# Optimization experiments

Measured on AMD Instinct MI355X. Metric: run time of the kernel, lower is better.

## Reference

```python
import jax, jax.numpy as jnp
import numpy as np

N_NODES, N_EDGES, NNZ, F_IN, HID, K = 50000, 10000, 800000, 128, 512, 10


def setup_inputs() -> dict:
    key = jax.random.key(0)
    ks = jax.random.split(key, 6)
    x = jax.random.normal(ks[0], (N_NODES, F_IN), dtype=jnp.float32)
    node_idx = jax.random.randint(ks[1], (NNZ,), 0, N_NODES)
    edge_idx = jax.random.randint(ks[2], (NNZ,), 0, N_EDGES)
    hyperedge_index = jnp.stack([node_idx, edge_idx]).astype(jnp.int64)
    edge_weight = jax.random.uniform(ks[3], (N_EDGES,), dtype=jnp.float32, minval=0.5, maxval=1.5)
    theta = jax.random.normal(ks[4], (K + 1,), dtype=jnp.float32) * 0.1
    lin1_w = jax.random.normal(ks[5], (HID, F_IN), dtype=jnp.float32) * (1.0 / np.sqrt(F_IN))
    lin1_b = jnp.zeros((HID,), dtype=jnp.float32)
    return {"x": x, "hyperedge_index": hyperedge_index, "edge_weight": edge_weight,
            "theta": theta, "lin1_w": lin1_w, "lin1_b": lin1_b}


def _hyper_prop_factory(node_idx, edge_idx, edge_weight, n_nodes, n_edges):
    """Returns A_norm @ x where A_norm = Dv^-1/2 H W De^-1 H^T Dv^-1/2."""
    ones = jnp.ones_like(node_idx, dtype=edge_weight.dtype)
    d_e = jax.ops.segment_sum(ones, edge_idx, num_segments=n_edges)            # edge degree
    d_v = jax.ops.segment_sum(edge_weight[edge_idx], node_idx, num_segments=n_nodes)
    dv_is = jnp.where(d_v > 0, jax.lax.rsqrt(jnp.maximum(d_v, 1e-12)), 0.0)
    de_w = edge_weight * jnp.where(d_e > 0, 1.0 / jnp.maximum(d_e, 1e-12), 0.0)

    def prop(x):
        xv = x * dv_is[:, None]                                               # [N, F]
        m_e = jax.ops.segment_sum(xv[node_idx], edge_idx, num_segments=n_edges)
        m_e = m_e * de_w[:, None]                                             # [E, F]
        out = jax.ops.segment_sum(m_e[edge_idx], node_idx, num_segments=n_nodes)
        return out * dv_is[:, None]

    return prop


def cheb_hypergraph(x, node_idx, edge_idx, edge_weight, theta, n_nodes, n_edges):
    # L_tilde = L - I = -A_norm (lambda_max = 2). Chebyshev recurrence on L_tilde.
    prop = _hyper_prop_factory(node_idx, edge_idx, edge_weight, n_nodes, n_edges)
    t_prev = x                       # T_0
    out = theta[0] * t_prev
    t_cur = -prop(x)                 # T_1 = L_tilde x
    out = out + theta[1] * t_cur
    for k in range(2, theta.shape[0]):
        t_next = -2.0 * prop(t_cur) - t_prev   # T_k = 2 L_tilde T_{k-1} - T_{k-2}
        out = out + theta[k] * t_next
        t_prev, t_cur = t_cur, t_next
    return out


def reference(x, hyperedge_index, edge_weight, theta, lin1_w, lin1_b):
    node_idx = hyperedge_index[0]
    edge_idx = hyperedge_index[1]
    n_nodes = x.shape[0]
    n_edges = edge_weight.shape[0]
    # eval mode: both dropouts are identity
    h = cheb_hypergraph(x, node_idx, edge_idx, edge_weight, theta, n_nodes, n_edges)
    h = jnp.einsum('nf,hf->nh', h, lin1_w) + lin1_b
    # is_bns=False -> no batch norm; act_fn='relu'
    return jax.nn.relu(h)
```

## Files before the change

kernel.cpp:

```cpp
#include <hip/hip_runtime.h>


#define N_NODES 50000
#define N_EDGES 10000
#define NNZ     800000
#define F_IN    128
#define HID     512
#define F4      (F_IN / 4)
#define R16     16

typedef __attribute__((ext_vector_type(8))) short bf16x8;
typedef __attribute__((ext_vector_type(4))) float f32x4;

static __device__ __forceinline__ unsigned short f2bf(float f) {
    union { float f; unsigned u; } c; c.f = f;
    unsigned u = c.u;
    unsigned r = (u + 0x7fffu + ((u >> 16) & 1u)) >> 16;
    return (unsigned short)r;
}
static __device__ __forceinline__ float blo(unsigned u) {
    union { unsigned u; float f; } c; c.u = u << 16; return c.f;
}
static __device__ __forceinline__ float bhi(unsigned u) {
    union { unsigned u; float f; } c; c.u = u & 0xffff0000u; return c.f;
}
static __device__ __forceinline__ unsigned pack2(float lo, float hi) {
    return (unsigned)f2bf(lo) | ((unsigned)f2bf(hi) << 16);
}

__global__ void k_zero8(int* __restrict__ cnt8_e, int* __restrict__ cnt8_n) {
    int i = blockIdx.x * blockDim.x + threadIdx.x;
    if (i < 8 * N_NODES) cnt8_n[i] = 0;
    if (i < 8 * N_EDGES) cnt8_e[i] = 0;
}

__global__ void k_degrees(const int* __restrict__ hidx,
                          int* __restrict__ cnt8_e,
                          int* __restrict__ cnt8_n,
                          int* __restrict__ rank_e,
                          int* __restrict__ rank_v) {
    int i = blockIdx.x * blockDim.x + threadIdx.x;
    if (i >= NNZ) return;
    int xcd = (int)blockIdx.x & 7;
    int v = hidx[i];
    int e = hidx[NNZ + i];
    v = min(max(v, 0), N_NODES - 1);
    e = min(max(e, 0), N_EDGES - 1);
    int re = atomicAdd(&cnt8_e[xcd * N_EDGES + e], 1);
    int rv = atomicAdd(&cnt8_n[xcd * N_NODES + v], 1);
    rank_e[i] = re | (xcd << 24);
    rank_v[i] = rv | (xcd << 24);
}

__global__ void k_off8(int* __restrict__ cnt8_e,
                       int* __restrict__ cnt8_n,
                       int* __restrict__ counts_e,
                       int* __restrict__ counts_n) {
    int i = blockIdx.x * blockDim.x + threadIdx.x;
    if (i < N_EDGES) {
        int s = 0;
#pragma unroll
        for (int x = 0; x < 8; ++x) {
            int c = cnt8_e[x * N_EDGES + i];
            cnt8_e[x * N_EDGES + i] = s;
            s += c;
        }
        counts_e[i] = s;
    }
    if (i < N_NODES) {
        int s = 0;
#pragma unroll
        for (int x = 0; x < 8; ++x) {
            int c = cnt8_n[x * N_NODES + i];
            cnt8_n[x * N_NODES + i] = s;
            s += c;
        }
        counts_n[i] = s;
    }
}

__global__ __launch_bounds__(1024) void k_scan_blk(const int* __restrict__ counts, int n,
                                                   int stride,
                                                   int* __restrict__ out,
                                                   int* __restrict__ partial) {
    __shared__ int sd[1024];
    int tid = (int)threadIdx.x;
    int i = blockIdx.x * 1024 + tid;
    int v = (i < n) ? counts[(size_t)i * stride] : 0;
    sd[tid] = v;
    __syncthreads();
    for (int off = 1; off < 1024; off <<= 1) {
        int t = (tid >= off) ? sd[tid - off] : 0;
        __syncthreads();
        sd[tid] += t;
        __syncthreads();
    }
    if (i < n) out[i] = sd[tid] - v;
    if (tid == 1023) partial[blockIdx.x] = sd[1023];
}

__global__ void k_scan_top(int* __restrict__ partial, int nb, int* __restrict__ total_out) {
    int lane = (int)threadIdx.x;
    int v = (lane < nb) ? partial[lane] : 0;
    int incl = v;
    for (int off = 1; off < 64; off <<= 1) {
        int t = __shfl_up(incl, off);
        if (lane >= off) incl += t;
    }
    if (lane < nb) partial[lane] = incl - v;
    if (lane == 63) *total_out = incl;
}

__global__ __launch_bounds__(1024) void k_scan_add(int* __restrict__ out, int n,
                                                   const int* __restrict__ partial) {
    int i = blockIdx.x * 1024 + (int)threadIdx.x;
    if (i < n) out[i] += partial[blockIdx.x];
}

__global__ void k_fill(const int* __restrict__ hidx,
                       const int* __restrict__ edge_ptr,
                       const int* __restrict__ node_ptr,
                       const int* __restrict__ rank_e,
                       const int* __restrict__ rank_v,
                       const int* __restrict__ off8_e,
                       const int* __restrict__ off8_n,
                       int* __restrict__ edge_node,
                       int* __restrict__ node_edge) {
    int i = blockIdx.x * blockDim.x + threadIdx.x;
    if (i >= NNZ) return;
    int v = hidx[i];
    int e = hidx[NNZ + i];
    v = min(max(v, 0), N_NODES - 1);
    e = min(max(e, 0), N_EDGES - 1);
    int pe = rank_e[i];
    int pv = rank_v[i];
    int xe = pe >> 24, re = pe & 0xFFFFFF;
    int xv = pv >> 24, rv = pv & 0xFFFFFF;
    edge_node[edge_ptr[e] + off8_e[xe * N_EDGES + e] + re] = v;
    node_edge[node_ptr[v] + off8_n[xv * N_NODES + v] + rv] = e;
}

__global__ void k_norms2(const float* __restrict__ ew,
                         const int* __restrict__ edge_ptr,
                         const int* __restrict__ node_ptr,
                         const int* __restrict__ node_edge,
                         float* __restrict__ dv_is,
                         float* __restrict__ de_w) {
    int i = blockIdx.x * blockDim.x + threadIdx.x;
    if (i < N_NODES) {
        int s = node_ptr[i], t = node_ptr[i + 1];
        float d = 0.f;
        for (int j = s; j < t; ++j) d += ew[node_edge[j]];
        dv_is[i] = (d > 0.f) ? rsqrtf(fmaxf(d, 1e-12f)) : 0.f;
    }
    if (i < N_EDGES) {
        int c = edge_ptr[i + 1] - edge_ptr[i];
        de_w[i] = ew[i] * ((c > 0) ? (1.f / (float)c) : 0.f);
    }
}

__global__ void k_init(const float* __restrict__ x,
                       const float* __restrict__ theta,
                       const float* __restrict__ dv_is,
                       uint4* __restrict__ bufA,
                       float* __restrict__ acc) {
    int i = blockIdx.x * blockDim.x + threadIdx.x;
    if (i >= N_NODES * R16) return;
    int v = i >> 4;
    float dvv = dv_is[v];
    float w = (dvv > 0.f) ? dvv : 1.f;
    float4 x0 = ((const float4*)x)[2 * i];
    float4 x1 = ((const float4*)x)[2 * i + 1];
    uint4 q;
    q.x = pack2(w * x0.x, w * x0.y); q.y = pack2(w * x0.z, w * x0.w);
    q.z = pack2(w * x1.x, w * x1.y); q.w = pack2(w * x1.z, w * x1.w);
    bufA[i] = q;
    float t0 = theta[0];
    float4 a0, a1;
    a0.x = t0 * x0.x; a0.y = t0 * x0.y; a0.z = t0 * x0.z; a0.w = t0 * x0.w;
    a1.x = t0 * x1.x; a1.y = t0 * x1.y; a1.z = t0 * x1.z; a1.w = t0 * x1.w;
    ((float4*)acc)[2 * i]     = a0;
    ((float4*)acc)[2 * i + 1] = a1;
}

__global__ void k_phaseA(const uint4* __restrict__ tin,
                         const float* __restrict__ de_w,
                         const int* __restrict__ edge_ptr,
                         const int* __restrict__ edge_node,
                         uint4* __restrict__ m_e) {
    int g      = threadIdx.x >> 5;
    int stream = (threadIdx.x >> 4) & 1;
    int lane   = threadIdx.x & 15;
    int e = blockIdx.x * 8 + g;
    int s = edge_ptr[e], t = edge_ptr[e + 1];
    float a0=0.f,a1=0.f,a2=0.f,a3=0.f,a4=0.f,a5=0.f,a6=0.f,a7=0.f;
    int j = s + stream;
    for (; j + 6 < t; j += 8) {
        int v0 = edge_node[j];
        int v1 = edge_node[j + 2];
        int v2 = edge_node[j + 4];
        int v3 = edge_node[j + 6];
        uint4 q0 = tin[v0 * R16 + lane];
        uint4 q1 = tin[v1 * R16 + lane];
        uint4 q2 = tin[v2 * R16 + lane];
        uint4 q3 = tin[v3 * R16 + lane];
        a0 += (blo(q0.x) + blo(q1.x)) + (blo(q2.x) + blo(q3.x));
        a1 += (bhi(q0.x) + bhi(q1.x)) + (bhi(q2.x) + bhi(q3.x));
        a2 += (blo(q0.y) + blo(q1.y)) + (blo(q2.y) + blo(q3.y));
        a3 += (bhi(q0.y) + bhi(q1.y)) + (bhi(q2.y) + bhi(q3.y));
        a4 += (blo(q0.z) + blo(q1.z)) + (blo(q2.z) + blo(q3.z));
        a5 += (bhi(q0.z) + bhi(q1.z)) + (bhi(q2.z) + bhi(q3.z));
        a6 += (blo(q0.w) + blo(q1.w)) + (blo(q2.w) + blo(q3.w));
        a7 += (bhi(q0.w) + bhi(q1.w)) + (bhi(q2.w) + bhi(q3.w));
    }
    for (; j < t; j += 2) {
        int v0 = edge_node[j];
        uint4 q0 = tin[v0 * R16 + lane];
        a0 += blo(q0.x); a1 += bhi(q0.x);
        a2 += blo(q0.y); a3 += bhi(q0.y);
        a4 += blo(q0.z); a5 += bhi(q0.z);
        a6 += blo(q0.w); a7 += bhi(q0.w);
    }
    a0 += __shfl_xor(a0, 16); a1 += __shfl_xor(a1, 16);
    a2 += __shfl_xor(a2, 16); a3 += __shfl_xor(a3, 16);
    a4 += __shfl_xor(a4, 16); a5 += __shfl_xor(a5, 16);
    a6 += __shfl_xor(a6, 16); a7 += __shfl_xor(a7, 16);
    if (stream == 0) {
        float w = de_w[e];
        uint4 o;
        o.x = pack2(a0 * w, a1 * w); o.y = pack2(a2 * w, a3 * w);
        o.z = pack2(a4 * w, a5 * w); o.w = pack2(a6 * w, a7 * w);
        m_e[e * R16 + lane] = o;
    }
}

__global__ void k_phaseB(const uint4* __restrict__ m_e,
                         const float* __restrict__ dv_is,
                         const int* __restrict__ node_ptr,
                         const int* __restrict__ node_edge,
                         uint4* __restrict__ tio,
                         float* __restrict__ acc,
                         const float* __restrict__ theta, int k,
                         float ca, float cb) {
    int g      = threadIdx.x >> 5;
    int stream = (threadIdx.x >> 4) & 1;
    int lane   = threadIdx.x & 15;
    int v = blockIdx.x * 8 + g;
    int s = node_ptr[v], t = node_ptr[v + 1];
    float s0=0.f,s1=0.f,s2=0.f,s3=0.f,s4=0.f,s5=0.f,s6=0.f,s7=0.f;
    int j = s + stream;
    for (; j + 2 < t; j += 4) {
        int e0 = node_edge[j];
        int e1 = node_edge[j + 2];
        uint4 q0 = m_e[e0 * R16 + lane];
        uint4 q1 = m_e[e1 * R16 + lane];
        s0 += blo(q0.x) + blo(q1.x); s1 += bhi(q0.x) + bhi(q1.x);
        s2 += blo(q0.y) + blo(q1.y); s3 += bhi(q0.y) + bhi(q1.y);
        s4 += blo(q0.z) + blo(q1.z); s5 += bhi(q0.z) + bhi(q1.z);
        s6 += blo(q0.w) + blo(q1.w); s7 += bhi(q0.w) + bhi(q1.w);
    }
    if (j < t) {
        int e0 = node_edge[j];
        uint4 q0 = m_e[e0 * R16 + lane];
        s0 += blo(q0.x); s1 += bhi(q0.x);
        s2 += blo(q0.y); s3 += bhi(q0.y);
        s4 += blo(q0.z); s5 += bhi(q0.z);
        s6 += blo(q0.w); s7 += bhi(q0.w);
    }
    s0 += __shfl_xor(s0, 16); s1 += __shfl_xor(s1, 16);
    s2 += __shfl_xor(s2, 16); s3 += __shfl_xor(s3, 16);
    s4 += __shfl_xor(s4, 16); s5 += __shfl_xor(s5, 16);
    s6 += __shfl_xor(s6, 16); s7 += __shfl_xor(s7, 16);
    if (stream == 0) {
        float dvv = dv_is[v];
        float scf = ca * dvv * dvv;
        float iw  = (dvv > 0.f) ? (1.f / dvv) : 1.f;
        float thinv = theta[k] * iw;
        int idx = v * R16 + lane;
        uint4 tp = tio[idx];
        float t0 = scf * s0 + cb * blo(tp.x);
        float t1 = scf * s1 + cb * bhi(tp.x);
        float t2 = scf * s2 + cb * blo(tp.y);
        float t3 = scf * s3 + cb * bhi(tp.y);
        float t4 = scf * s4 + cb * blo(tp.z);
        float t5 = scf * s5 + cb * bhi(tp.z);
        float t6 = scf * s6 + cb * blo(tp.w);
        float t7 = scf * s7 + cb * bhi(tp.w);
        uint4 tn;
        tn.x = pack2(t0, t1); tn.y = pack2(t2, t3);
        tn.z = pack2(t4, t5); tn.w = pack2(t6, t7);
        tio[idx] = tn;
        float4* acc4 = (float4*)acc;
        int ai = v * 32 + lane * 2;
        float4 a = acc4[ai];
        a.x += thinv * t0; a.y += thinv * t1; a.z += thinv * t2; a.w += thinv * t3;
        acc4[ai] = a;
        float4 b = acc4[ai + 1];
        b.x += thinv * t4; b.y += thinv * t5; b.z += thinv * t6; b.w += thinv * t7;
        acc4[ai + 1] = b;
    }
}

#define M_TILES 782
__global__ __launch_bounds__(256) void k_gemm(const float* __restrict__ A,
                                              const float* __restrict__ W,
                                              const float* __restrict__ bias,
                                              float* __restrict__ out) {
    __shared__ short Asm[64 * 136];
    __shared__ short Wsm[64 * 136];
    int id  = (int)blockIdx.x;
    int xcd = id & 7;
    int sub = id >> 3;
    int h_t = sub & 7;
    int m_i = sub >> 3;
    int m_t = xcd * 98 + m_i;
    if (m_t >= M_TILES) return;
    int m0 = m_t * 64;
    int h0 = h_t * 64;
    int tid = (int)threadIdx.x;

    const float4* A4 = (const float4*)A;
    const float4* W4 = (const float4*)W;
#pragma unroll
    for (int i = 0; i < 4; ++i) {
        int c   = tid + i * 256;
        int row = c >> 4;
        int q4  = c & 15;
        int gr = m0 + row;
        float4 a0, a1;
        if (gr < N_NODES) {
            a0 = A4[(size_t)gr * 32 + q4 * 2];
            a1 = A4[(size_t)gr * 32 + q4 * 2 + 1];
        } else {
            a0 = make_float4(0.f, 0.f, 0.f, 0.f);
            a1 = a0;
        }
        uint4 pa;
        pa.x = pack2(a0.x, a0.y); pa.y = pack2(a0.z, a0.w);
        pa.z = pack2(a1.x, a1.y); pa.w = pack2(a1.z, a1.w);
        *(uint4*)&Asm[row * 136 + q4 * 8] = pa;
        float4 w0 = W4[(size_t)(h0 + row) * 32 + q4 * 2];
        float4 w1 = W4[(size_t)(h0 + row) * 32 + q4 * 2 + 1];
        uint4 pw;
        pw.x = pack2(w0.x, w0.y); pw.y = pack2(w0.z, w0.w);
        pw.z = pack2(w1.x, w1.y); pw.w = pack2(w1.z, w1.w);
        *(uint4*)&Wsm[row * 136 + q4 * 8] = pw;
    }
    __syncthreads();

    int lane = tid & 63;
    int wv   = tid >> 6;
    int l16  = lane & 15;
    int quad = lane >> 4;

    f32x4 acc[4];
#pragma unroll
    for (int n = 0; n < 4; ++n) acc[n] = (f32x4){0.f, 0.f, 0.f, 0.f};

#pragma unroll
    for (int ks = 0; ks < 4; ++ks) {
        int k0 = ks * 32;
        bf16x8 af = *(const bf16x8*)&Asm[(wv * 16 + l16) * 136 + k0 + quad * 8];
#pragma unroll
        for (int n = 0; n < 4; ++n) {
            bf16x8 bf = *(const bf16x8*)&Wsm[(n * 16 + l16) * 136 + k0 + quad * 8];
            acc[n] = __builtin_amdgcn_mfma_f32_16x16x32_bf16(af, bf, acc[n], 0, 0, 0);
        }
    }

#pragma unroll
    for (int n = 0; n < 4; ++n) {
        float bb = bias[h0 + n * 16 + l16];
#pragma unroll
        for (int r = 0; r < 4; ++r) {
            int gr = m0 + wv * 16 + quad * 4 + r;
            if (gr < N_NODES)
                out[(size_t)gr * HID + h0 + n * 16 + l16] =
                    fmaxf(acc[n][r] + bb, 0.f);
        }
    }
}

extern "C" void kernel_launch(void* const* d_in, const int* in_sizes, int n_in,
                              void* d_out, int out_size, void* d_ws, size_t ws_size,
                              hipStream_t stream) {
    const float* x     = (const float*)d_in[0];
    const int*   hidx  = (const int*)d_in[1];
    const float* ew    = (const float*)d_in[2];
    const float* theta = (const float*)d_in[3];
    const float* w1    = (const float*)d_in[4];
    const float* b1    = (const float*)d_in[5];
    float*       out   = (float*)d_out;
    int kp1 = in_sizes[3];

    char* ob = (char*)d_out;
    size_t oo = 0;
    auto oalloc = [&](size_t bytes) -> void* {
        void* p = ob + oo;
        oo = (oo + bytes + 255) & ~(size_t)255;
        return p;
    };
    uint4* bufA      = (uint4*)oalloc((size_t)N_NODES * F_IN * 2);
    uint4* bufB      = (uint4*)oalloc((size_t)N_NODES * F_IN * 2);
    uint4* m_e       = (uint4*)oalloc((size_t)N_EDGES * F_IN * 2);
    int*   edge_node = (int*)oalloc((size_t)NNZ * 4);
    int*   node_edge = (int*)oalloc((size_t)NNZ * 4);
    int*   rank_e    = (int*)oalloc((size_t)NNZ * 4);
    int*   rank_v    = (int*)oalloc((size_t)NNZ * 4);
    int*   cnt8_e    = (int*)oalloc((size_t)8 * N_EDGES * 4);
    int*   cnt8_n    = (int*)oalloc((size_t)8 * N_NODES * 4);
    int*   counts_e  = (int*)oalloc((size_t)N_EDGES * 4);
    int*   counts_n  = (int*)oalloc((size_t)N_NODES * 4);

    char* ws = (char*)d_ws;
    size_t off = 0;
    auto alloc = [&](size_t bytes) -> void* {
        void* p = ws + off;
        off = (off + bytes + 255) & ~(size_t)255;
        return p;
    };
    float* accv     = (float*)alloc((size_t)N_NODES * F_IN * 4);
    float* dv_is    = (float*)alloc((size_t)N_NODES * 4);
    float* de_w     = (float*)alloc((size_t)N_EDGES * 4);
    int*   edge_ptr = (int*)alloc((size_t)(N_EDGES + 1) * 4);
    int*   node_ptr = (int*)alloc((size_t)(N_NODES + 1) * 4);
    int*   part_e   = (int*)alloc(64 * 4);
    int*   part_n   = (int*)alloc(64 * 4);

    const int NB_E = (N_EDGES + 1023) / 1024;
    const int NB_N = (N_NODES + 1023) / 1024;

    k_zero8<<<(8 * N_NODES + 255) / 256, 256, 0, stream>>>(cnt8_e, cnt8_n);
    k_degrees<<<(NNZ + 255) / 256, 256, 0, stream>>>(hidx, cnt8_e, cnt8_n, rank_e, rank_v);
    k_off8<<<(N_NODES + 255) / 256, 256, 0, stream>>>(cnt8_e, cnt8_n, counts_e, counts_n);

    k_scan_blk<<<NB_E, 1024, 0, stream>>>(counts_e, N_EDGES, 1, edge_ptr, part_e);
    k_scan_top<<<1, 64, 0, stream>>>(part_e, NB_E, edge_ptr + N_EDGES);
    k_scan_add<<<NB_E, 1024, 0, stream>>>(edge_ptr, N_EDGES, part_e);

    k_scan_blk<<<NB_N, 1024, 0, stream>>>(counts_n, N_NODES, 1, node_ptr, part_n);
    k_scan_top<<<1, 64, 0, stream>>>(part_n, NB_N, node_ptr + N_NODES);
    k_scan_add<<<NB_N, 1024, 0, stream>>>(node_ptr, N_NODES, part_n);

    k_fill<<<(NNZ + 255) / 256, 256, 0, stream>>>(hidx, edge_ptr, node_ptr,
                                                  rank_e, rank_v, cnt8_e, cnt8_n,
                                                  edge_node, node_edge);
    k_norms2<<<(N_NODES + 255) / 256, 256, 0, stream>>>(ew, edge_ptr, node_ptr,
                                                        node_edge, dv_is, de_w);
    k_init<<<(N_NODES * R16 + 255) / 256, 256, 0, stream>>>(x, theta, dv_is, bufA, accv);

    for (int k = 1; k < kp1; ++k) {
        const uint4* tin = (k & 1) ? bufA : bufB;
        uint4*       tio = (k & 1) ? bufB : bufA;
        float ca = (k == 1) ? -1.f : -2.f;
        float cb = (k == 1) ? 0.f : -1.f;
        k_phaseA<<<N_EDGES / 8, 256, 0, stream>>>(tin, de_w, edge_ptr, edge_node, m_e);
        k_phaseB<<<N_NODES / 8, 256, 0, stream>>>(m_e, dv_is, node_ptr, node_edge,
                                                  tio, accv, theta, k, ca, cb);
    }

    k_gemm<<<8 * 98 * 8, 256, 0, stream>>>(accv, w1, b1, out);
}
```

Baseline: 796.3 us.

## Batch Chebyshev accumulator updates every three steps, widen phaseA, merge scans

The fp32 accumulator read-modify-write in phaseB now runs only every third Chebyshev step, plus the final step. It folds theta-weighted contributions of the current, previous (tin) and pre-previous (tio before overwrite) bf16 terms, which removes about two thirds of the full-size accumulator traffic. phaseA now assigns 64 threads (four interleaved streams) per hyperedge instead of 32, adding a second shuffle reduction, to raise memory-level parallelism per edge. The separate edge and node prefix-scan kernels are merged into single launches to cut launch overhead. The trade-off is that older terms are accumulated from bf16-rounded values rather than fp32, a small precision change.

```diff
diff --git a/kernel.cpp b/kernel.cpp
--- a/kernel.cpp
+++ b/kernel.cpp
@@ -8,6 +8,8 @@
 #define HID     512
 #define F4      (F_IN / 4)
 #define R16     16
+#define NB_E    10
+#define NB_N    49
 
 typedef __attribute__((ext_vector_type(8))) short bf16x8;
 typedef __attribute__((ext_vector_type(4))) float f32x4;
@@ -79,14 +81,20 @@
     }
 }
 
-__global__ __launch_bounds__(1024) void k_scan_blk(const int* __restrict__ counts, int n,
-                                                   int stride,
-                                                   int* __restrict__ out,
-                                                   int* __restrict__ partial) {
+__global__ __launch_bounds__(1024) void k_scan_blk2(const int* __restrict__ ce,
+                                                    const int* __restrict__ cn,
+                                                    int* __restrict__ oute,
+                                                    int* __restrict__ outn,
+                                                    int* __restrict__ pe,
+                                                    int* __restrict__ pn) {
     __shared__ int sd[1024];
+    int b = (int)blockIdx.x;
+    const int* counts; int n; int* out; int* partial; int lb;
+    if (b < NB_E) { counts = ce; n = N_EDGES; out = oute; partial = pe; lb = b; }
+    else          { counts = cn; n = N_NODES; out = outn; partial = pn; lb = b - NB_E; }
     int tid = (int)threadIdx.x;
-    int i = blockIdx.x * 1024 + tid;
-    int v = (i < n) ? counts[(size_t)i * stride] : 0;
+    int i = lb * 1024 + tid;
+    int v = (i < n) ? counts[i] : 0;
     sd[tid] = v;
     __syncthreads();
     for (int off = 1; off < 1024; off <<= 1) {
@@ -96,11 +104,16 @@
         __syncthreads();
     }
     if (i < n) out[i] = sd[tid] - v;
-    if (tid == 1023) partial[blockIdx.x] = sd[1023];
-}
-
-__global__ void k_scan_top(int* __restrict__ partial, int nb, int* __restrict__ total_out) {
-    int lane = (int)threadIdx.x;
+    if (tid == 1023) partial[lb] = sd[1023];
+}
+
+__global__ void k_scan_top2(int* __restrict__ pe, int* __restrict__ pn,
+                            int* __restrict__ tot_e, int* __restrict__ tot_n) {
+    int w = (int)threadIdx.x >> 6;
+    int lane = (int)threadIdx.x & 63;
+    int* partial = w ? pn : pe;
+    int nb       = w ? NB_N : NB_E;
+    int* total   = w ? tot_n : tot_e;
     int v = (lane < nb) ? partial[lane] : 0;
     int incl = v;
     for (int off = 1; off < 64; off <<= 1) {
@@ -108,13 +121,19 @@
         if (lane >= off) incl += t;
     }
     if (lane < nb) partial[lane] = incl - v;
-    if (lane == 63) *total_out = incl;
-}
-
-__global__ __launch_bounds__(1024) void k_scan_add(int* __restrict__ out, int n,
-                                                   const int* __restrict__ partial) {
-    int i = blockIdx.x * 1024 + (int)threadIdx.x;
-    if (i < n) out[i] += partial[blockIdx.x];
+    if (lane == 63) *total = incl;
+}
+
+__global__ __launch_bounds__(1024) void k_scan_add2(int* __restrict__ oute,
+                                                    int* __restrict__ outn,
+                                                    const int* __restrict__ pe,
+                                                    const int* __restrict__ pn) {
+    int b = (int)blockIdx.x;
+    int* out; const int* partial; int n; int lb;
+    if (b < NB_E) { out = oute; partial = pe; n = N_EDGES; lb = b; }
+    else          { out = outn; partial = pn; n = N_NODES; lb = b - NB_E; }
+    int i = lb * 1024 + (int)threadIdx.x;
+    if (i < n) out[i] += partial[lb];
 }
 
 __global__ void k_fill(const int* __restrict__ hidx,
@@ -188,18 +207,20 @@
                          const int* __restrict__ edge_ptr,
                          const int* __restrict__ edge_node,
                          uint4* __restrict__ m_e) {
-    int g      = threadIdx.x >> 5;
-    int stream = (threadIdx.x >> 4) & 1;
-    int lane   = threadIdx.x & 15;
-    int e = blockIdx.x * 8 + g;
+    int tid    = (int)threadIdx.x;
+    int g      = tid >> 6;
+    int l64    = tid & 63;
+    int stream = l64 >> 4;
+    int lane   = l64 & 15;
+    int e = blockIdx.x * 4 + g;
     int s = edge_ptr[e], t = edge_ptr[e + 1];
     float a0=0.f,a1=0.f,a2=0.f,a3=0.f,a4=0.f,a5=0.f,a6=0.f,a7=0.f;
     int j = s + stream;
-    for (; j + 6 < t; j += 8) {
+    for (; j + 12 < t; j += 16) {
         int v0 = edge_node[j];
-        int v1 = edge_node[j + 2];
-        int v2 = edge_node[j + 4];
-        int v3 = edge_node[j + 6];
+        int v1 = edge_node[j + 4];
+        int v2 = edge_node[j + 8];
+        int v3 = edge_node[j + 12];
         uint4 q0 = tin[v0 * R16 + lane];
         uint4 q1 = tin[v1 * R16 + lane];
         uint4 q2 = tin[v2 * R16 + lane];
@@ -213,7 +234,7 @@
         a6 += (blo(q0.w) + blo(q1.w)) + (blo(q2.w) + blo(q3.w));
         a7 += (bhi(q0.w) + bhi(q1.w)) + (bhi(q2.w) + bhi(q3.w));
     }
-    for (; j < t; j += 2) {
+    for (; j < t; j += 4) {
         int v0 = edge_node[j];
         uint4 q0 = tin[v0 * R16 + lane];
         a0 += blo(q0.x); a1 += bhi(q0.x);
@@ -225,6 +246,10 @@
     a2 += __shfl_xor(a2, 16); a3 += __shfl_xor(a3, 16);
     a4 += __shfl_xor(a4, 16); a5 += __shfl_xor(a5, 16);
     a6 += __shfl_xor(a6, 16); a7 += __shfl_xor(a7, 16);
+    a0 += __shfl_xor(a0, 32); a1 += __shfl_xor(a1, 32);
+    a2 += __shfl_xor(a2, 32); a3 += __shfl_xor(a3, 32);
+    a4 += __shfl_xor(a4, 32); a5 += __shfl_xor(a5, 32);
+    a6 += __shfl_xor(a6, 32); a7 += __shfl_xor(a7, 32);
     if (stream == 0) {
         float w = de_w[e];
         uint4 o;
@@ -235,13 +260,14 @@
 }
 
 __global__ void k_phaseB(const uint4* __restrict__ m_e,
+                         const uint4* __restrict__ tin,
                          const float* __restrict__ dv_is,
                          const int* __restrict__ node_ptr,
                          const int* __restrict__ node_edge,
                          uint4* __restrict__ tio,
                          float* __restrict__ acc,
                          const float* __restrict__ theta, int k,
-                         float ca, float cb) {
+                         float ca, float cb, int accMode) {
     int g      = threadIdx.x >> 5;
     int stream = (threadIdx.x >> 4) & 1;
     int lane   = threadIdx.x & 15;
@@ -274,8 +300,6 @@
     if (stream == 0) {
         float dvv = dv_is[v];
         float scf = ca * dvv * dvv;
-        float iw  = (dvv > 0.f) ? (1.f / dvv) : 1.f;
-        float thinv = theta[k] * iw;
         int idx = v * R16 + lane;
         uint4 tp = tio[idx];
         float t0 = scf * s0 + cb * blo(tp.x);
@@ -290,14 +314,35 @@
         tn.x = pack2(t0, t1); tn.y = pack2(t2, t3);
         tn.z = pack2(t4, t5); tn.w = pack2(t6, t7);
         tio[idx] = tn;
-        float4* acc4 = (float4*)acc;
-        int ai = v * 32 + lane * 2;
-        float4 a = acc4[ai];
-        a.x += thinv * t0; a.y += thinv * t1; a.z += thinv * t2; a.w += thinv * t3;
-        acc4[ai] = a;
-        float4 b = acc4[ai + 1];
-        b.x += thinv * t4; b.y += thinv * t5; b.z += thinv * t6; b.w += thinv * t7;
-        acc4[ai + 1] = b;
+        if (accMode) {
+            float thk = theta[k];
+            float a0 = thk * t0, a1 = thk * t1, a2 = thk * t2, a3 = thk * t3;
+            float a4 = thk * t4, a5 = thk * t5, a6 = thk * t6, a7 = thk * t7;
+            if (accMode >= 2) {
+                float th1 = theta[k - 1];
+                uint4 tq = tin[idx];
+                a0 += th1 * blo(tq.x); a1 += th1 * bhi(tq.x);
+                a2 += th1 * blo(tq.y); a3 += th1 * bhi(tq.y);
+                a4 += th1 * blo(tq.z); a5 += th1 * bhi(tq.z);
+                a6 += th1 * blo(tq.w); a7 += th1 * bhi(tq.w);
+            }
+            if (accMode >= 3) {
+                float th2 = theta[k - 2];
+                a0 += th2 * blo(tp.x); a1 += th2 * bhi(tp.x);
+                a2 += th2 * blo(tp.y); a3 += th2 * bhi(tp.y);
+                a4 += th2 * blo(tp.z); a5 += th2 * bhi(tp.z);
+                a6 += th2 * blo(tp.w); a7 += th2 * bhi(tp.w);
+            }
+            float iw = (dvv > 0.f) ? (1.f / dvv) : 1.f;
+            float4* acc4 = (float4*)acc;
+            int ai = v * 32 + lane * 2;
+            float4 a = acc4[ai];
+            a.x += iw * a0; a.y += iw * a1; a.z += iw * a2; a.w += iw * a3;
+            acc4[ai] = a;
+            float4 b = acc4[ai + 1];
+            b.x += iw * a4; b.y += iw * a5; b.z += iw * a6; b.w += iw * a7;
+            acc4[ai + 1] = b;
+        }
     }
 }
 
@@ -392,6 +437,7 @@
     const float* b1    = (const float*)d_in[5];
     float*       out   = (float*)d_out;
     int kp1 = in_sizes[3];
+    int K   = kp1 - 1;
 
     char* ob = (char*)d_out;
     size_t oo = 0;
@@ -427,20 +473,14 @@
     int*   part_e   = (int*)alloc(64 * 4);
     int*   part_n   = (int*)alloc(64 * 4);
 
-    const int NB_E = (N_EDGES + 1023) / 1024;
-    const int NB_N = (N_NODES + 1023) / 1024;
-
     k_zero8<<<(8 * N_NODES + 255) / 256, 256, 0, stream>>>(cnt8_e, cnt8_n);
     k_degrees<<<(NNZ + 255) / 256, 256, 0, stream>>>(hidx, cnt8_e, cnt8_n, rank_e, rank_v);
     k_off8<<<(N_NODES + 255) / 256, 256, 0, stream>>>(cnt8_e, cnt8_n, counts_e, counts_n);
 
-    k_scan_blk<<<NB_E, 1024, 0, stream>>>(counts_e, N_EDGES, 1, edge_ptr, part_e);
-    k_scan_top<<<1, 64, 0, stream>>>(part_e, NB_E, edge_ptr + N_EDGES);
-    k_scan_add<<<NB_E, 1024, 0, stream>>>(edge_ptr, N_EDGES, part_e);
-
-    k_scan_blk<<<NB_N, 1024, 0, stream>>>(counts_n, N_NODES, 1, node_ptr, part_n);
-    k_scan_top<<<1, 64, 0, stream>>>(part_n, NB_N, node_ptr + N_NODES);
-    k_scan_add<<<NB_N, 1024, 0, stream>>>(node_ptr, N_NODES, part_n);
+    k_scan_blk2<<<NB_E + NB_N, 1024, 0, stream>>>(counts_e, counts_n, edge_ptr, node_ptr,
+                                                  part_e, part_n);
+    k_scan_top2<<<1, 128, 0, stream>>>(part_e, part_n, edge_ptr + N_EDGES, node_ptr + N_NODES);
+    k_scan_add2<<<NB_E + NB_N, 1024, 0, stream>>>(edge_ptr, node_ptr, part_e, part_n);
 
     k_fill<<<(NNZ + 255) / 256, 256, 0, stream>>>(hidx, edge_ptr, node_ptr,
                                                   rank_e, rank_v, cnt8_e, cnt8_n,
@@ -449,14 +489,17 @@
                                                         node_edge, dv_is, de_w);
     k_init<<<(N_NODES * R16 + 255) / 256, 256, 0, stream>>>(x, theta, dv_is, bufA, accv);
 
-    for (int k = 1; k < kp1; ++k) {
+    for (int k = 1; k <= K; ++k) {
         const uint4* tin = (k & 1) ? bufA : bufB;
         uint4*       tio = (k & 1) ? bufB : bufA;
         float ca = (k == 1) ? -1.f : -2.f;
         float cb = (k == 1) ? 0.f : -1.f;
-        k_phaseA<<<N_EDGES / 8, 256, 0, stream>>>(tin, de_w, edge_ptr, edge_node, m_e);
-        k_phaseB<<<N_NODES / 8, 256, 0, stream>>>(m_e, dv_is, node_ptr, node_edge,
-                                                  tio, accv, theta, k, ca, cb);
+        int accMode = 0;
+        if (k % 3 == 0) accMode = 3;
+        else if (k == K && (K % 3) != 0) accMode = K % 3;
+        k_phaseA<<<N_EDGES / 4, 256, 0, stream>>>(tin, de_w, edge_ptr, edge_node, m_e);
+        k_phaseB<<<N_NODES / 8, 256, 0, stream>>>(m_e, tin, dv_is, node_ptr, node_edge,
+                                                  tio, accv, theta, k, ca, cb, accMode);
     }
 
     k_gemm<<<8 * 98 * 8, 256, 0, stream>>>(accv, w1, b1, out);
```

Result: faster. 774.2 us (-2.8%).
